# Kernel tuning notes

Measured on AMD Instinct MI355X. Metric: run time of the kernel, lower is better.

Reference implementation:

```python
import jax, jax.numpy as jnp
import numpy as np

P, E, D = 128, 32, 64          # n_proxy_sets, n_elements, d
B, SEG_LEN = 1024, 128          # number of segments, per-segment length
N = B * SEG_LEN                 # total elements


def setup_inputs() -> dict:
    key = jax.random.key(0)
    k_x, k_p = jax.random.split(key)
    x = jax.random.normal(k_x, (N, D), dtype=jnp.float32)
    proxy_sets = jax.random.normal(k_p, (P, E, D), dtype=jnp.float32)
    index = jnp.full((B,), SEG_LEN, dtype=jnp.int32)  # segment lengths, sum == N
    return {"x": x, "proxy_sets": proxy_sets, "index": index}


def reference(x, proxy_sets, index):
    # sim_mat[p,e,n] = proxy_sets[p,e,:] . x[n,:]
    sim = jnp.einsum("ped,nd->pen", proxy_sets, x)     # [P,E,N]
    t = jnp.max(sim, axis=1)                             # [P,N]  max over proxy elements
    # ragged segment sum over N driven by segment lengths `index`
    seg_ids = jnp.repeat(jnp.arange(B, dtype=jnp.int32), index,
                         total_repeat_length=N)          # [N]
    pooled = jax.ops.segment_sum(t.T, seg_ids, num_segments=B)  # [B,P]
    pooled = pooled.astype(jnp.float32)
    # F.normalize(p=2, dim=1): divide by max(||.||_2, eps)
    norm = jnp.linalg.norm(pooled, axis=1, keepdims=True)
    return pooled / jnp.maximum(norm, 1e-12)
```

## Files before the change

kernel.cpp:

```cpp
#include <hip/hip_runtime.h>
#include <stdint.h>


typedef short short8 __attribute__((ext_vector_type(8)));
typedef __bf16 bf16x8 __attribute__((ext_vector_type(8)));
typedef float floatx16 __attribute__((ext_vector_type(16)));

#define NELEM 32
#define DIM   64
#define NSEG  1024
#define BROW  36

__device__ __forceinline__ unsigned short f32_to_bf16_rne(float f) {
  union { float f; unsigned int u; } v; v.f = f;
  unsigned int r = v.u + 0x7fffu + ((v.u >> 16) & 1u);
  return (unsigned short)(r >> 16);
}

__global__ void sc_prep(const float* __restrict__ proxy,
                        const int* __restrict__ index,
                        short* __restrict__ pb2,
                        int* __restrict__ offs) {
  const int bx = blockIdx.x, t = threadIdx.x;
  if (bx == 0) {
    __shared__ int lsum[256];
    const int base = t * 4;
    const int i0 = index[base + 0], i1 = index[base + 1];
    const int i2 = index[base + 2], i3 = index[base + 3];
    const int s = i0 + i1 + i2 + i3;
    lsum[t] = s;
    __syncthreads();
    for (int off = 1; off < 256; off <<= 1) {
      int v = (t >= off) ? lsum[t - off] : 0;
      __syncthreads();
      lsum[t] += v;
      __syncthreads();
    }
    const int ex = lsum[t] - s;
    offs[base + 0] = ex;
    offs[base + 1] = ex + i0;
    offs[base + 2] = ex + i0 + i1;
    offs[base + 3] = ex + i0 + i1 + i2;
    if (t == 255) offs[NSEG] = ex + s;
  } else {
    const int w = t >> 6, lane = t & 63;
    const int task = (bx - 1) * 4 + w;
    const int p = task >> 2, kk = task & 3;
    const int l31 = lane & 31, h = lane >> 5;
    const float* src = proxy + (size_t)p * (NELEM * DIM) + l31 * DIM + kk * 16 + h * 8;
    float4 f0 = *(const float4*)(src);
    float4 f1 = *(const float4*)(src + 4);
    short8 fr;
    fr[0] = (short)f32_to_bf16_rne(f0.x);
    fr[1] = (short)f32_to_bf16_rne(f0.y);
    fr[2] = (short)f32_to_bf16_rne(f0.z);
    fr[3] = (short)f32_to_bf16_rne(f0.w);
    fr[4] = (short)f32_to_bf16_rne(f1.x);
    fr[5] = (short)f32_to_bf16_rne(f1.y);
    fr[6] = (short)f32_to_bf16_rne(f1.z);
    fr[7] = (short)f32_to_bf16_rne(f1.w);
    *(short8*)(pb2 + ((size_t)task * 64 + lane) * 8) = fr;
  }
}

__device__ __forceinline__ float max16(const floatx16& a) {
  float r0 = fmaxf(fmaxf(a[0], a[1]), a[2]);
  float r1 = fmaxf(fmaxf(a[3], a[4]), a[5]);
  float r2 = fmaxf(fmaxf(a[6], a[7]), a[8]);
  float r3 = fmaxf(fmaxf(a[9], a[10]), a[11]);
  float r4 = fmaxf(fmaxf(a[12], a[13]), a[14]);
  float r5 = fmaxf(fmaxf(r0, r1), r2);
  float r6 = fmaxf(fmaxf(r3, r4), a[15]);
  return fmaxf(r5, r6);
}

__global__ __launch_bounds__(256, 2) void sc_main(
    const float* __restrict__ x,
    const short* __restrict__ pb2,
    const int* __restrict__ offs,
    float* __restrict__ out,
    int nrows) {
  __shared__ float buf[128 * BROW];
  __shared__ float red[4];

  const int b = blockIdx.x;
  const int tid = threadIdx.x;
  const int lane = tid & 63;
  const int w = tid >> 6;
  const int l31 = lane & 31;
  const int h = lane >> 5;

  const int start = offs[b];
  const int end = offs[b + 1];
  const int len = end - start;
  const int first = start >> 5;
  const int ntiles = (len > 0) ? (((end + 31) >> 5) - first) : 0;
  const int npass = (ntiles + 3) >> 2;

  if (ntiles == 0) {
    for (int j = tid; j < 128 * BROW; j += 256) buf[j] = 0.f;
  }

  floatx16 zc;
#pragma unroll
  for (int r = 0; r < 16; ++r) zc[r] = 0.f;

  const short* abase = pb2 + ((size_t)w * 4 * 64 + lane) * 8;

  for (int pass = 0; pass < npass; ++pass) {
    short8 bfrag[4][4];
    bool vmask[4];
#pragma unroll
    for (int t4 = 0; t4 < 4; ++t4) {
      const int tile = first + pass * 4 + t4;
      const int n = tile * 32 + l31;
      vmask[t4] = (n >= start) && (n < end);
      int rn = n < nrows ? n : nrows - 1;
      const float* xr = x + (size_t)rn * DIM + h * 8;
#pragma unroll
      for (int kk = 0; kk < 4; ++kk) {
        float4 f0 = *(const float4*)(xr + kk * 16);
        float4 f1 = *(const float4*)(xr + kk * 16 + 4);
        short8 fr;
        fr[0] = (short)f32_to_bf16_rne(f0.x);
        fr[1] = (short)f32_to_bf16_rne(f0.y);
        fr[2] = (short)f32_to_bf16_rne(f0.z);
        fr[3] = (short)f32_to_bf16_rne(f0.w);
        fr[4] = (short)f32_to_bf16_rne(f1.x);
        fr[5] = (short)f32_to_bf16_rne(f1.y);
        fr[6] = (short)f32_to_bf16_rne(f1.z);
        fr[7] = (short)f32_to_bf16_rne(f1.w);
        bfrag[t4][kk] = fr;
      }
    }

    auto process = [&](int i, short8 (&cur)[4], short8 (&nxt)[4], bool pf) {
      if (pf) {
        const short* ap = abase + (size_t)(i + 1) * 8192;
#pragma unroll
        for (int kk = 0; kk < 4; ++kk)
          nxt[kk] = *(const short8*)(ap + kk * 512);
      }
      floatx16 a0, a1, a2, a3;
#pragma unroll
      for (int kk = 0; kk < 4; ++kk) {
        bf16x8 a = __builtin_bit_cast(bf16x8, cur[kk]);
        bf16x8 b0 = __builtin_bit_cast(bf16x8, bfrag[0][kk]);
        bf16x8 b1 = __builtin_bit_cast(bf16x8, bfrag[1][kk]);
        bf16x8 b2 = __builtin_bit_cast(bf16x8, bfrag[2][kk]);
        bf16x8 b3 = __builtin_bit_cast(bf16x8, bfrag[3][kk]);
        if (kk == 0) {
          a0 = __builtin_amdgcn_mfma_f32_32x32x16_bf16(a, b0, zc, 0, 0, 0);
          a1 = __builtin_amdgcn_mfma_f32_32x32x16_bf16(a, b1, zc, 0, 0, 0);
          a2 = __builtin_amdgcn_mfma_f32_32x32x16_bf16(a, b2, zc, 0, 0, 0);
          a3 = __builtin_amdgcn_mfma_f32_32x32x16_bf16(a, b3, zc, 0, 0, 0);
        } else {
          a0 = __builtin_amdgcn_mfma_f32_32x32x16_bf16(a, b0, a0, 0, 0, 0);
          a1 = __builtin_amdgcn_mfma_f32_32x32x16_bf16(a, b1, a1, 0, 0, 0);
          a2 = __builtin_amdgcn_mfma_f32_32x32x16_bf16(a, b2, a2, 0, 0, 0);
          a3 = __builtin_amdgcn_mfma_f32_32x32x16_bf16(a, b3, a3, 0, 0, 0);
        }
      }
      float m0 = max16(a0), m1 = max16(a1), m2 = max16(a2), m3 = max16(a3);
      m0 = fmaxf(m0, __shfl_xor(m0, 32, 64));
      m1 = fmaxf(m1, __shfl_xor(m1, 32, 64));
      m2 = fmaxf(m2, __shfl_xor(m2, 32, 64));
      m3 = fmaxf(m3, __shfl_xor(m3, 32, 64));
      m0 = vmask[0] ? m0 : 0.f;
      m1 = vmask[1] ? m1 : 0.f;
      m2 = vmask[2] ? m2 : 0.f;
      m3 = vmask[3] ? m3 : 0.f;
      const float s = (m0 + m1) + (m2 + m3);
      if (h == 0) {
        const int p = w + 4 * i;
        const int idx = p * BROW + l31;
        float prev = (pass == 0) ? 0.f : buf[idx];
        buf[idx] = prev + s;
      }
    };

    short8 afA[4], afB[4];
#pragma unroll
    for (int kk = 0; kk < 4; ++kk)
      afA[kk] = *(const short8*)(abase + kk * 512);
    for (int i = 0; i < 32; i += 2) {
      process(i, afA, afB, true);
      process(i + 1, afB, afA, i < 30);
    }
  }
  __syncthreads();

  const int p2 = tid >> 1, part = tid & 1;
  const float* bp = buf + p2 * BROW + part * 16;
  float4 v0 = *(const float4*)(bp + 0);
  float4 v1 = *(const float4*)(bp + 4);
  float4 v2 = *(const float4*)(bp + 8);
  float4 v3 = *(const float4*)(bp + 12);
  float s16 = ((v0.x + v0.y) + (v0.z + v0.w)) + ((v1.x + v1.y) + (v1.z + v1.w)) +
              ((v2.x + v2.y) + (v2.z + v2.w)) + ((v3.x + v3.y) + (v3.z + v3.w));
  const float s32 = s16 + __shfl_xor(s16, 1, 64);

  float sq = part ? 0.f : s32 * s32;
#pragma unroll
  for (int off = 1; off <= 32; off <<= 1) sq += __shfl_xor(sq, off, 64);
  if (lane == 0) red[w] = sq;
  __syncthreads();
  const float ss = (red[0] + red[1]) + (red[2] + red[3]);
  const float inv = 1.f / fmaxf(sqrtf(ss), 1e-12f);
  if (part == 0) out[(b << 7) + p2] = s32 * inv;
}

extern "C" void kernel_launch(void* const* d_in, const int* in_sizes, int n_in,
                              void* d_out, int out_size, void* d_ws, size_t ws_size,
                              hipStream_t stream) {
  (void)n_in; (void)out_size; (void)ws_size;
  const float* x = (const float*)d_in[0];
  const float* proxy = (const float*)d_in[1];
  const int* index = (const int*)d_in[2];
  float* out = (float*)d_out;
  const int nrows = in_sizes[0] / DIM;

  int* offs = (int*)d_ws;
  short* pb2 = (short*)((char*)d_ws + 8192);

  sc_prep<<<129, 256, 0, stream>>>(proxy, index, pb2, offs);
  sc_main<<<NSEG, 256, 0, stream>>>(x, pb2, offs, out, nrows);
}
```

Baseline: 136.9 us.

## Split waves across tile pairs and proxy halves, raise occupancy to four blocks

Each wave now covers two of the four row tiles and 64 of the 128 proxy sets, instead of all four tiles and 32 proxy sets. This halves the per-wave B-fragment registers and accumulators, so launch bounds can ask for four blocks per CU. Out-of-segment rows are now skipped with predicated zero loads rather than masked after the max. The cost is a larger LDS buffer (128x68 floats) and twice as many A-fragment loads per wave per pass, since each wave iterates 64 proxy sets.

```diff
diff --git a/kernel.cpp b/kernel.cpp
--- a/kernel.cpp
+++ b/kernel.cpp
@@ -9,7 +9,7 @@
 #define NELEM 32
 #define DIM   64
 #define NSEG  1024
-#define BROW  36
+#define LROW  68
 
 __device__ __forceinline__ unsigned short f32_to_bf16_rne(float f) {
   union { float f; unsigned int u; } v; v.f = f;
@@ -74,19 +74,21 @@
   return fmaxf(r5, r6);
 }
 
-__global__ __launch_bounds__(256, 2) void sc_main(
+__global__ __launch_bounds__(256, 4) void sc_main(
     const float* __restrict__ x,
     const short* __restrict__ pb2,
     const int* __restrict__ offs,
     float* __restrict__ out,
     int nrows) {
-  __shared__ float buf[128 * BROW];
+  __shared__ float buf[128 * LROW];
   __shared__ float red[4];
 
   const int b = blockIdx.x;
   const int tid = threadIdx.x;
   const int lane = tid & 63;
   const int w = tid >> 6;
+  const int wn = w & 1;
+  const int wp = w >> 1;
   const int l31 = lane & 31;
   const int h = lane >> 5;
 
@@ -98,29 +100,30 @@
   const int npass = (ntiles + 3) >> 2;
 
   if (ntiles == 0) {
-    for (int j = tid; j < 128 * BROW; j += 256) buf[j] = 0.f;
+    for (int j = tid; j < 128 * LROW; j += 256) buf[j] = 0.f;
   }
 
   floatx16 zc;
 #pragma unroll
   for (int r = 0; r < 16; ++r) zc[r] = 0.f;
 
-  const short* abase = pb2 + ((size_t)w * 4 * 64 + lane) * 8;
+  const short* abase = pb2 + (size_t)(wp * 64) * 2048 + lane * 8;
 
   for (int pass = 0; pass < npass; ++pass) {
-    short8 bfrag[4][4];
-    bool vmask[4];
-#pragma unroll
-    for (int t4 = 0; t4 < 4; ++t4) {
-      const int tile = first + pass * 4 + t4;
+    short8 bfrag[2][4];
+#pragma unroll
+    for (int t4 = 0; t4 < 2; ++t4) {
+      const int tile = first + pass * 4 + wn * 2 + t4;
       const int n = tile * 32 + l31;
-      vmask[t4] = (n >= start) && (n < end);
-      int rn = n < nrows ? n : nrows - 1;
-      const float* xr = x + (size_t)rn * DIM + h * 8;
+      const bool valid = (n >= start) && (n < end) && (n < nrows);
+      const float* xr = x + (size_t)(valid ? n : 0) * DIM + h * 8;
 #pragma unroll
       for (int kk = 0; kk < 4; ++kk) {
-        float4 f0 = *(const float4*)(xr + kk * 16);
-        float4 f1 = *(const float4*)(xr + kk * 16 + 4);
+        float4 f0 = make_float4(0.f, 0.f, 0.f, 0.f), f1 = f0;
+        if (valid) {
+          f0 = *(const float4*)(xr + kk * 16);
+          f1 = *(const float4*)(xr + kk * 16 + 4);
+        }
         short8 fr;
         fr[0] = (short)f32_to_bf16_rne(f0.x);
         fr[1] = (short)f32_to_bf16_rne(f0.y);
@@ -136,44 +139,31 @@
 
     auto process = [&](int i, short8 (&cur)[4], short8 (&nxt)[4], bool pf) {
       if (pf) {
-        const short* ap = abase + (size_t)(i + 1) * 8192;
+        const short* ap = abase + (size_t)(i + 1) * 2048;
 #pragma unroll
         for (int kk = 0; kk < 4; ++kk)
           nxt[kk] = *(const short8*)(ap + kk * 512);
       }
-      floatx16 a0, a1, a2, a3;
+      floatx16 a0, a1;
 #pragma unroll
       for (int kk = 0; kk < 4; ++kk) {
         bf16x8 a = __builtin_bit_cast(bf16x8, cur[kk]);
         bf16x8 b0 = __builtin_bit_cast(bf16x8, bfrag[0][kk]);
         bf16x8 b1 = __builtin_bit_cast(bf16x8, bfrag[1][kk]);
-        bf16x8 b2 = __builtin_bit_cast(bf16x8, bfrag[2][kk]);
-        bf16x8 b3 = __builtin_bit_cast(bf16x8, bfrag[3][kk]);
         if (kk == 0) {
           a0 = __builtin_amdgcn_mfma_f32_32x32x16_bf16(a, b0, zc, 0, 0, 0);
           a1 = __builtin_amdgcn_mfma_f32_32x32x16_bf16(a, b1, zc, 0, 0, 0);
-          a2 = __builtin_amdgcn_mfma_f32_32x32x16_bf16(a, b2, zc, 0, 0, 0);
-          a3 = __builtin_amdgcn_mfma_f32_32x32x16_bf16(a, b3, zc, 0, 0, 0);
         } else {
           a0 = __builtin_amdgcn_mfma_f32_32x32x16_bf16(a, b0, a0, 0, 0, 0);
           a1 = __builtin_amdgcn_mfma_f32_32x32x16_bf16(a, b1, a1, 0, 0, 0);
-          a2 = __builtin_amdgcn_mfma_f32_32x32x16_bf16(a, b2, a2, 0, 0, 0);
-          a3 = __builtin_amdgcn_mfma_f32_32x32x16_bf16(a, b3, a3, 0, 0, 0);
         }
       }
-      float m0 = max16(a0), m1 = max16(a1), m2 = max16(a2), m3 = max16(a3);
+      float m0 = max16(a0), m1 = max16(a1);
       m0 = fmaxf(m0, __shfl_xor(m0, 32, 64));
       m1 = fmaxf(m1, __shfl_xor(m1, 32, 64));
-      m2 = fmaxf(m2, __shfl_xor(m2, 32, 64));
-      m3 = fmaxf(m3, __shfl_xor(m3, 32, 64));
-      m0 = vmask[0] ? m0 : 0.f;
-      m1 = vmask[1] ? m1 : 0.f;
-      m2 = vmask[2] ? m2 : 0.f;
-      m3 = vmask[3] ? m3 : 0.f;
-      const float s = (m0 + m1) + (m2 + m3);
+      const float s = m0 + m1;
       if (h == 0) {
-        const int p = w + 4 * i;
-        const int idx = p * BROW + l31;
+        const int idx = (wp * 64 + i) * LROW + wn * 32 + l31;
         float prev = (pass == 0) ? 0.f : buf[idx];
         buf[idx] = prev + s;
       }
@@ -183,31 +173,37 @@
 #pragma unroll
     for (int kk = 0; kk < 4; ++kk)
       afA[kk] = *(const short8*)(abase + kk * 512);
-    for (int i = 0; i < 32; i += 2) {
+    for (int i = 0; i < 64; i += 2) {
       process(i, afA, afB, true);
-      process(i + 1, afB, afA, i < 30);
+      process(i + 1, afB, afA, i < 62);
     }
   }
   __syncthreads();
 
   const int p2 = tid >> 1, part = tid & 1;
-  const float* bp = buf + p2 * BROW + part * 16;
+  const float* bp = buf + p2 * LROW + part * 32;
   float4 v0 = *(const float4*)(bp + 0);
   float4 v1 = *(const float4*)(bp + 4);
   float4 v2 = *(const float4*)(bp + 8);
   float4 v3 = *(const float4*)(bp + 12);
-  float s16 = ((v0.x + v0.y) + (v0.z + v0.w)) + ((v1.x + v1.y) + (v1.z + v1.w)) +
-              ((v2.x + v2.y) + (v2.z + v2.w)) + ((v3.x + v3.y) + (v3.z + v3.w));
-  const float s32 = s16 + __shfl_xor(s16, 1, 64);
-
-  float sq = part ? 0.f : s32 * s32;
+  float4 v4 = *(const float4*)(bp + 16);
+  float4 v5 = *(const float4*)(bp + 20);
+  float4 v6 = *(const float4*)(bp + 24);
+  float4 v7 = *(const float4*)(bp + 28);
+  float sh = ((v0.x + v0.y) + (v0.z + v0.w)) + ((v1.x + v1.y) + (v1.z + v1.w)) +
+             ((v2.x + v2.y) + (v2.z + v2.w)) + ((v3.x + v3.y) + (v3.z + v3.w)) +
+             ((v4.x + v4.y) + (v4.z + v4.w)) + ((v5.x + v5.y) + (v5.z + v5.w)) +
+             ((v6.x + v6.y) + (v6.z + v6.w)) + ((v7.x + v7.y) + (v7.z + v7.w));
+  const float s64 = sh + __shfl_xor(sh, 1, 64);
+
+  float sq = part ? 0.f : s64 * s64;
 #pragma unroll
   for (int off = 1; off <= 32; off <<= 1) sq += __shfl_xor(sq, off, 64);
   if (lane == 0) red[w] = sq;
   __syncthreads();
   const float ss = (red[0] + red[1]) + (red[2] + red[3]);
   const float inv = 1.f / fmaxf(sqrtf(ss), 1e-12f);
-  if (part == 0) out[(b << 7) + p2] = s32 * inv;
+  if (part == 0) out[(b << 7) + p2] = s64 * inv;
 }
 
 extern "C" void kernel_launch(void* const* d_in, const int* in_sizes, int n_in,
```

After: 138.0 us. Within noise of the previous version (+0.8%).

## Reorder proxy layout so MFMA rows span proxy sets and max is elementwise

Applied to the files above, without the earlier changes.

Proxy fragments are reordered so each MFMA A-tile holds 32 different proxy sets for one element. The max over elements then becomes an elementwise fmax across iterations on the accumulator registers, replacing the per-tile 16-way max tree plus cross-half shuffle. Invalid rows are zero-filled rather than masked after the max. This keeps four persistent 16-float max accumulators live, which adds register pressure and could hurt occupancy.

```diff
diff --git a/kernel.cpp b/kernel.cpp
--- a/kernel.cpp
+++ b/kernel.cpp
@@ -19,7 +19,7 @@
 
 __global__ void sc_prep(const float* __restrict__ proxy,
                         const int* __restrict__ index,
-                        short* __restrict__ pb2,
+                        short* __restrict__ pa2,
                         int* __restrict__ offs) {
   const int bx = blockIdx.x, t = threadIdx.x;
   if (bx == 0) {
@@ -43,11 +43,11 @@
     offs[base + 3] = ex + i0 + i1 + i2;
     if (t == 255) offs[NSEG] = ex + s;
   } else {
-    const int w = t >> 6, lane = t & 63;
-    const int task = (bx - 1) * 4 + w;
-    const int p = task >> 2, kk = task & 3;
+    const int wv = t >> 6, lane = t & 63;
+    const int f = (bx - 1) * 4 + wv;
+    const int g = f >> 7, e = (f >> 2) & 31, kk = f & 3;
     const int l31 = lane & 31, h = lane >> 5;
-    const float* src = proxy + (size_t)p * (NELEM * DIM) + l31 * DIM + kk * 16 + h * 8;
+    const float* src = proxy + ((size_t)(g * 32 + l31) * NELEM + e) * DIM + kk * 16 + h * 8;
     float4 f0 = *(const float4*)(src);
     float4 f1 = *(const float4*)(src + 4);
     short8 fr;
@@ -59,24 +59,13 @@
     fr[5] = (short)f32_to_bf16_rne(f1.y);
     fr[6] = (short)f32_to_bf16_rne(f1.z);
     fr[7] = (short)f32_to_bf16_rne(f1.w);
-    *(short8*)(pb2 + ((size_t)task * 64 + lane) * 8) = fr;
+    *(short8*)(pa2 + ((size_t)f * 64 + lane) * 8) = fr;
   }
-}
-
-__device__ __forceinline__ float max16(const floatx16& a) {
-  float r0 = fmaxf(fmaxf(a[0], a[1]), a[2]);
-  float r1 = fmaxf(fmaxf(a[3], a[4]), a[5]);
-  float r2 = fmaxf(fmaxf(a[6], a[7]), a[8]);
-  float r3 = fmaxf(fmaxf(a[9], a[10]), a[11]);
-  float r4 = fmaxf(fmaxf(a[12], a[13]), a[14]);
-  float r5 = fmaxf(fmaxf(r0, r1), r2);
-  float r6 = fmaxf(fmaxf(r3, r4), a[15]);
-  return fmaxf(r5, r6);
 }
 
 __global__ __launch_bounds__(256, 2) void sc_main(
     const float* __restrict__ x,
-    const short* __restrict__ pb2,
+    const short* __restrict__ pa2,
     const int* __restrict__ offs,
     float* __restrict__ out,
     int nrows) {
@@ -86,7 +75,7 @@
   const int b = blockIdx.x;
   const int tid = threadIdx.x;
   const int lane = tid & 63;
-  const int w = tid >> 6;
+  const int g = tid >> 6;
   const int l31 = lane & 31;
   const int h = lane >> 5;
 
@@ -105,22 +94,22 @@
 #pragma unroll
   for (int r = 0; r < 16; ++r) zc[r] = 0.f;
 
-  const short* abase = pb2 + ((size_t)w * 4 * 64 + lane) * 8;
+  const short* abase = pa2 + (size_t)g * (128 * 512) + lane * 8;
 
   for (int pass = 0; pass < npass; ++pass) {
     short8 bfrag[4][4];
-    bool vmask[4];
 #pragma unroll
     for (int t4 = 0; t4 < 4; ++t4) {
-      const int tile = first + pass * 4 + t4;
-      const int n = tile * 32 + l31;
-      vmask[t4] = (n >= start) && (n < end);
-      int rn = n < nrows ? n : nrows - 1;
-      const float* xr = x + (size_t)rn * DIM + h * 8;
+      const int n = (first + pass * 4 + t4) * 32 + l31;
+      const bool valid = (n >= start) && (n < end) && (n < nrows);
+      const float* xr = x + (size_t)(valid ? n : 0) * DIM + h * 8;
 #pragma unroll
       for (int kk = 0; kk < 4; ++kk) {
-        float4 f0 = *(const float4*)(xr + kk * 16);
-        float4 f1 = *(const float4*)(xr + kk * 16 + 4);
+        float4 f0 = make_float4(0.f, 0.f, 0.f, 0.f), f1 = f0;
+        if (valid) {
+          f0 = *(const float4*)(xr + kk * 16);
+          f1 = *(const float4*)(xr + kk * 16 + 4);
+        }
         short8 fr;
         fr[0] = (short)f32_to_bf16_rne(f0.x);
         fr[1] = (short)f32_to_bf16_rne(f0.y);
@@ -134,58 +123,79 @@
       }
     }
 
-    auto process = [&](int i, short8 (&cur)[4], short8 (&nxt)[4], bool pf) {
+    floatx16 M0, M1, M2, M3;
+#pragma unroll
+    for (int r = 0; r < 16; ++r) {
+      M0[r] = -3.0e38f; M1[r] = -3.0e38f; M2[r] = -3.0e38f; M3[r] = -3.0e38f;
+    }
+
+    auto estep = [&](const short8 (&cur)[4], short8 (&nxt)[4], int enext, bool pf) {
       if (pf) {
-        const short* ap = abase + (size_t)(i + 1) * 8192;
+        const short* ap = abase + (size_t)enext * 2048;
 #pragma unroll
         for (int kk = 0; kk < 4; ++kk)
           nxt[kk] = *(const short8*)(ap + kk * 512);
       }
-      floatx16 a0, a1, a2, a3;
-#pragma unroll
-      for (int kk = 0; kk < 4; ++kk) {
-        bf16x8 a = __builtin_bit_cast(bf16x8, cur[kk]);
-        bf16x8 b0 = __builtin_bit_cast(bf16x8, bfrag[0][kk]);
-        bf16x8 b1 = __builtin_bit_cast(bf16x8, bfrag[1][kk]);
-        bf16x8 b2 = __builtin_bit_cast(bf16x8, bfrag[2][kk]);
-        bf16x8 b3 = __builtin_bit_cast(bf16x8, bfrag[3][kk]);
-        if (kk == 0) {
-          a0 = __builtin_amdgcn_mfma_f32_32x32x16_bf16(a, b0, zc, 0, 0, 0);
-          a1 = __builtin_amdgcn_mfma_f32_32x32x16_bf16(a, b1, zc, 0, 0, 0);
-          a2 = __builtin_amdgcn_mfma_f32_32x32x16_bf16(a, b2, zc, 0, 0, 0);
-          a3 = __builtin_amdgcn_mfma_f32_32x32x16_bf16(a, b3, zc, 0, 0, 0);
-        } else {
-          a0 = __builtin_amdgcn_mfma_f32_32x32x16_bf16(a, b0, a0, 0, 0, 0);
-          a1 = __builtin_amdgcn_mfma_f32_32x32x16_bf16(a, b1, a1, 0, 0, 0);
-          a2 = __builtin_amdgcn_mfma_f32_32x32x16_bf16(a, b2, a2, 0, 0, 0);
-          a3 = __builtin_amdgcn_mfma_f32_32x32x16_bf16(a, b3, a3, 0, 0, 0);
-        }
-      }
-      float m0 = max16(a0), m1 = max16(a1), m2 = max16(a2), m3 = max16(a3);
-      m0 = fmaxf(m0, __shfl_xor(m0, 32, 64));
-      m1 = fmaxf(m1, __shfl_xor(m1, 32, 64));
-      m2 = fmaxf(m2, __shfl_xor(m2, 32, 64));
-      m3 = fmaxf(m3, __shfl_xor(m3, 32, 64));
-      m0 = vmask[0] ? m0 : 0.f;
-      m1 = vmask[1] ? m1 : 0.f;
-      m2 = vmask[2] ? m2 : 0.f;
-      m3 = vmask[3] ? m3 : 0.f;
-      const float s = (m0 + m1) + (m2 + m3);
-      if (h == 0) {
-        const int p = w + 4 * i;
-        const int idx = p * BROW + l31;
-        float prev = (pass == 0) ? 0.f : buf[idx];
-        buf[idx] = prev + s;
+      {
+        floatx16 d0, d1;
+#pragma unroll
+        for (int kk = 0; kk < 4; ++kk) {
+          bf16x8 a = __builtin_bit_cast(bf16x8, cur[kk]);
+          bf16x8 b0 = __builtin_bit_cast(bf16x8, bfrag[0][kk]);
+          bf16x8 b1 = __builtin_bit_cast(bf16x8, bfrag[1][kk]);
+          if (kk == 0) {
+            d0 = __builtin_amdgcn_mfma_f32_32x32x16_bf16(a, b0, zc, 0, 0, 0);
+            d1 = __builtin_amdgcn_mfma_f32_32x32x16_bf16(a, b1, zc, 0, 0, 0);
+          } else {
+            d0 = __builtin_amdgcn_mfma_f32_32x32x16_bf16(a, b0, d0, 0, 0, 0);
+            d1 = __builtin_amdgcn_mfma_f32_32x32x16_bf16(a, b1, d1, 0, 0, 0);
+          }
+        }
+#pragma unroll
+        for (int r = 0; r < 16; ++r) {
+          M0[r] = fmaxf(M0[r], d0[r]);
+          M1[r] = fmaxf(M1[r], d1[r]);
+        }
+      }
+      {
+        floatx16 d0, d1;
+#pragma unroll
+        for (int kk = 0; kk < 4; ++kk) {
+          bf16x8 a = __builtin_bit_cast(bf16x8, cur[kk]);
+          bf16x8 b2 = __builtin_bit_cast(bf16x8, bfrag[2][kk]);
+          bf16x8 b3 = __builtin_bit_cast(bf16x8, bfrag[3][kk]);
+          if (kk == 0) {
+            d0 = __builtin_amdgcn_mfma_f32_32x32x16_bf16(a, b2, zc, 0, 0, 0);
+            d1 = __builtin_amdgcn_mfma_f32_32x32x16_bf16(a, b3, zc, 0, 0, 0);
+          } else {
+            d0 = __builtin_amdgcn_mfma_f32_32x32x16_bf16(a, b2, d0, 0, 0, 0);
+            d1 = __builtin_amdgcn_mfma_f32_32x32x16_bf16(a, b3, d1, 0, 0, 0);
+          }
+        }
+#pragma unroll
+        for (int r = 0; r < 16; ++r) {
+          M2[r] = fmaxf(M2[r], d0[r]);
+          M3[r] = fmaxf(M3[r], d1[r]);
+        }
       }
     };
 
-    short8 afA[4], afB[4];
+    short8 aA[4], aB[4];
 #pragma unroll
     for (int kk = 0; kk < 4; ++kk)
-      afA[kk] = *(const short8*)(abase + kk * 512);
-    for (int i = 0; i < 32; i += 2) {
-      process(i, afA, afB, true);
-      process(i + 1, afB, afA, i < 30);
+      aA[kk] = *(const short8*)(abase + kk * 512);
+    for (int e = 0; e < 32; e += 2) {
+      estep(aA, aB, e + 1, true);
+      estep(aB, aA, e + 2, e < 30);
+    }
+
+#pragma unroll
+    for (int r = 0; r < 16; ++r) {
+      const float s = (M0[r] + M1[r]) + (M2[r] + M3[r]);
+      const int p = g * 32 + (r & 3) + 8 * (r >> 2) + 4 * h;
+      const int idx = p * BROW + l31;
+      const float prev = (pass == 0) ? 0.f : buf[idx];
+      buf[idx] = prev + s;
     }
   }
   __syncthreads();
@@ -203,7 +213,7 @@
   float sq = part ? 0.f : s32 * s32;
 #pragma unroll
   for (int off = 1; off <= 32; off <<= 1) sq += __shfl_xor(sq, off, 64);
-  if (lane == 0) red[w] = sq;
+  if (lane == 0) red[tid >> 6] = sq;
   __syncthreads();
   const float ss = (red[0] + red[1]) + (red[2] + red[3]);
   const float inv = 1.f / fmaxf(sqrtf(ss), 1e-12f);
@@ -221,8 +231,8 @@
   const int nrows = in_sizes[0] / DIM;
 
   int* offs = (int*)d_ws;
-  short* pb2 = (short*)((char*)d_ws + 8192);
-
-  sc_prep<<<129, 256, 0, stream>>>(proxy, index, pb2, offs);
-  sc_main<<<NSEG, 256, 0, stream>>>(x, pb2, offs, out, nrows);
-}
+  short* pa2 = (short*)((char*)d_ws + 8192);
+
+  sc_prep<<<129, 256, 0, stream>>>(proxy, index, pa2, offs);
+  sc_main<<<NSEG, 256, 0, stream>>>(x, pa2, offs, out, nrows);
+}
```

Measured after the change: 146.3 us. +6.9%, slower.
